# Kernel optimization log

Hardware: AMD Instinct MI355X
Metric: run time of the kernel (lower is better)

## Reference

```python
import jax, jax.numpy as jnp
import numpy as np

D_MODEL = 1024
N_HEADS = 16
SEQ = 2048
BATCH = 2


def setup_inputs() -> dict:
    key = jax.random.key(0)
    ks = jax.random.split(key, 12)
    s = 1.0 / np.sqrt(D_MODEL)
    return {
        "q_input": jax.random.normal(ks[0], (BATCH, SEQ, D_MODEL), jnp.float32),
        "k_input": jax.random.normal(ks[1], (BATCH, SEQ, D_MODEL), jnp.float32),
        "v_input": jax.random.normal(ks[2], (BATCH, SEQ, D_MODEL), jnp.float32),
        "key_padding_mask": jnp.zeros((BATCH, SEQ), dtype=bool),
        "wq": jax.random.normal(ks[3], (D_MODEL, D_MODEL), jnp.float32) * s,
        "bq": jnp.zeros((D_MODEL,), jnp.float32),
        "wk": jax.random.normal(ks[4], (D_MODEL, D_MODEL), jnp.float32) * s,
        "bk": jnp.zeros((D_MODEL,), jnp.float32),
        "wv": jax.random.normal(ks[5], (D_MODEL, D_MODEL), jnp.float32) * s,
        "bv": jnp.zeros((D_MODEL,), jnp.float32),
        "wo": jax.random.normal(ks[6], (D_MODEL, D_MODEL), jnp.float32) * s,
        "bo": jnp.zeros((D_MODEL,), jnp.float32),
    }


def reference(q_input, k_input, v_input, key_padding_mask, wq, bq, wk, bk, wv, bv, wo, bo):
    B, Lq, _ = q_input.shape
    Lk = k_input.shape[1]
    d_head = D_MODEL // N_HEADS
    # torch Linear: x @ W.T + b
    Q = q_input @ wq.T + bq
    K = k_input @ wk.T + bk
    V = v_input @ wv.T + bv
    # [B, H, L, d_head]
    Qh = Q.reshape(B, Lq, N_HEADS, d_head).transpose(0, 2, 1, 3)
    Kh = K.reshape(B, Lk, N_HEADS, d_head).transpose(0, 2, 1, 3)
    Vh = V.reshape(B, Lk, N_HEADS, d_head).transpose(0, 2, 1, 3)
    scores = jnp.einsum("bhqd,bhkd->bhqk", Qh, Kh) / jnp.sqrt(jnp.float32(d_head))
    # causal mask (use_mask=True)
    causal = jnp.arange(Lk)[None, :] > jnp.arange(Lq)[:, None]  # [Lq, Lk]
    scores = jnp.where(causal[None, None], -jnp.inf, scores)
    # key padding mask [B,1,1,Lk]
    scores = jnp.where(key_padding_mask[:, None, None, :], -jnp.inf, scores)
    # module's global all-inf fallback (scalar condition)
    probs = jnp.where(
        jnp.all(jnp.isinf(scores)),
        jnp.full_like(scores, 1.0 / Lk),
        jax.nn.softmax(scores, axis=-1),
    )
    # dropout is identity in eval mode
    out = jnp.einsum("bhqk,bhkd->bhqd", probs, Vh)
    out = out.transpose(0, 2, 1, 3).reshape(B, Lq, D_MODEL)
    return out @ wo.T + bo
```

## Files before the change

### kernel.cpp

```cpp
#include <hip/hip_runtime.h>
#include <cstdint>
#include <cstddef>

#define DM   1024
#define HEADS 16
#define DH    64
#define SEQL  2048
#define BATCH 2
#define MTOT  (BATCH*SEQL)

typedef __attribute__((ext_vector_type(8))) short short8;
typedef __attribute__((ext_vector_type(4))) float floatx4;

__device__ __forceinline__ unsigned short f2bf(float f) {
  unsigned int u = __float_as_uint(f);
  u = (u + 0x7FFFu + ((u >> 16) & 1u)) >> 16;
  return (unsigned short)u;
}

__device__ __forceinline__ void async_ld16(const void* g, void* l) {
  __builtin_amdgcn_global_load_lds(
      (const __attribute__((address_space(1))) unsigned int*)g,
      (__attribute__((address_space(3))) unsigned int*)l, 16, 0, 0);
}

__global__ void cvt_all(const float* __restrict__ q, const float* __restrict__ k,
                        const float* __restrict__ v, const float* __restrict__ w0,
                        const float* __restrict__ w1, const float* __restrict__ w2,
                        const float* __restrict__ w3,
                        unsigned short* __restrict__ Xq, unsigned short* __restrict__ Xk,
                        unsigned short* __restrict__ Xv, unsigned short* __restrict__ W0,
                        unsigned short* __restrict__ W1, unsigned short* __restrict__ W2,
                        unsigned short* __restrict__ W3) {
  const int bid = blockIdx.x;
  const float* src; unsigned short* dst; int base;
  if (bid < 12288) {
    int seg = bid >> 12;
    base = (bid & 4095) * 1024;
    src = seg == 0 ? q : seg == 1 ? k : v;
    dst = seg == 0 ? Xq : seg == 1 ? Xk : Xv;
  } else {
    int b2 = bid - 12288;
    int seg = b2 >> 10;
    base = (b2 & 1023) * 1024;
    src = seg == 0 ? w0 : seg == 1 ? w1 : seg == 2 ? w2 : w3;
    dst = seg == 0 ? W0 : seg == 1 ? W1 : seg == 2 ? W2 : W3;
  }
  int i = base + threadIdx.x * 4;
  float4 vv = *(const float4*)(src + i);
  ushort4 o;
  o.x = f2bf(vv.x); o.y = f2bf(vv.y); o.z = f2bf(vv.z); o.w = f2bf(vv.w);
  *(ushort4*)(dst + i) = o;
}

__global__ __launch_bounds__(256, 3) void qkv_gemm(
    const unsigned short* Xq, const unsigned short* Xk, const unsigned short* Xv,
    const unsigned short* Wq, const unsigned short* Wk, const unsigned short* Wv,
    const float* bq, const float* bk, const float* bv,
    unsigned short* Qo, unsigned short* Ko, unsigned short* VTo) {
  __shared__ unsigned short As[128 * 64], Bs[128 * 64];
  const unsigned short *A, *Bw; const float* bias; unsigned short* Cout;
  if (blockIdx.z == 0)      { A = Xq; Bw = Wq; bias = bq; Cout = Qo; }
  else if (blockIdx.z == 1) { A = Xk; Bw = Wk; bias = bk; Cout = Ko; }
  else                      { A = Xv; Bw = Wv; bias = bv; Cout = VTo; }

  const int K = DM, N = DM;
  const int m0 = blockIdx.y * 128, n0 = blockIdx.x * 128;
  const int tid  = threadIdx.x;
  const int lane = tid & 63, wvi = tid >> 6;
  const int lq = lane & 15, quad = lane >> 4;
  const int wrow = wvi >> 1, wcol = wvi & 1;

  floatx4 acc[4][4];
  #pragma unroll
  for (int i = 0; i < 4; i++)
    #pragma unroll
    for (int j = 0; j < 4; j++)
      #pragma unroll
      for (int e = 0; e < 4; e++) acc[i][j][e] = 0.0f;

  for (int kt = 0; kt < K; kt += 64) {
    #pragma unroll
    for (int cc = 0; cc < 4; cc++) {
      int c = wvi + cc * 4;
      int e = c * 512 + lane * 8;
      int r = e >> 6, col = e & 63;
      async_ld16(A  + (size_t)(m0 + r) * K + kt + col, As + c * 512);
      async_ld16(Bw + (size_t)(n0 + r) * K + kt + col, Bs + c * 512);
    }
    __syncthreads();
    #pragma unroll
    for (int ks = 0; ks < 64; ks += 32) {
      short8 af[4], bf[4];
      #pragma unroll
      for (int i = 0; i < 4; i++)
        af[i] = *(const short8*)&As[(wrow * 64 + i * 16 + lq) * 64 + ks + quad * 8];
      #pragma unroll
      for (int j = 0; j < 4; j++)
        bf[j] = *(const short8*)&Bs[(wcol * 64 + j * 16 + lq) * 64 + ks + quad * 8];
      #pragma unroll
      for (int i = 0; i < 4; i++)
        #pragma unroll
        for (int j = 0; j < 4; j++)
          acc[i][j] = __builtin_amdgcn_mfma_f32_16x16x32_bf16(af[i], bf[j], acc[i][j], 0, 0, 0);
    }
    __syncthreads();
  }

  if (blockIdx.z == 2) {
    #pragma unroll
    for (int i = 0; i < 4; i++) {
      const int rowg = m0 + wrow * 64 + i * 16 + quad * 4;
      const int bb  = rowg >> 11;
      const int kt2 = (rowg & 2047) >> 6;
      const int k0  = rowg & 63;
      #pragma unroll
      for (int j = 0; j < 4; j++) {
        const int colg = n0 + wcol * 64 + j * 16 + lq;
        const int h2 = colg >> 6, d2 = colg & 63;
        const float bb_v = bias[colg];
        ushort4 w;
        w.x = f2bf(acc[i][j][0] + bb_v);
        w.y = f2bf(acc[i][j][1] + bb_v);
        w.z = f2bf(acc[i][j][2] + bb_v);
        w.w = f2bf(acc[i][j][3] + bb_v);
        *(ushort4*)(Cout + (size_t)((bb * HEADS + h2) * 32 + kt2) * 4096 + d2 * 64 + k0) = w;
      }
    }
  } else {
    #pragma unroll
    for (int i = 0; i < 4; i++) {
      #pragma unroll
      for (int j = 0; j < 4; j++) {
        int colg = n0 + wcol * 64 + j * 16 + lq;
        float bb = bias[colg];
        #pragma unroll
        for (int r = 0; r < 4; r++) {
          int rowg = m0 + wrow * 64 + i * 16 + quad * 4 + r;
          Cout[(size_t)rowg * N + colg] = f2bf(acc[i][j][r] + bb);
        }
      }
    }
  }
}

__global__ __launch_bounds__(256, 4) void out_gemm(
    const unsigned short* __restrict__ A, const unsigned short* __restrict__ Bw,
    const float* __restrict__ bias, float* __restrict__ C) {
  __shared__ unsigned short As[128 * 64], Bs[64 * 64];
  const int K = DM, N = DM;
  const int m0 = blockIdx.y * 128, n0 = blockIdx.x * 64;
  const int tid  = threadIdx.x;
  const int lane = tid & 63, wvi = tid >> 6;
  const int lq = lane & 15, quad = lane >> 4;
  const int wrow = wvi >> 1, wcol = wvi & 1;

  floatx4 acc[4][2];
  #pragma unroll
  for (int i = 0; i < 4; i++)
    #pragma unroll
    for (int j = 0; j < 2; j++)
      #pragma unroll
      for (int e = 0; e < 4; e++) acc[i][j][e] = 0.0f;

  for (int kt = 0; kt < K; kt += 64) {
    #pragma unroll
    for (int cc = 0; cc < 4; cc++) {
      int c = wvi + cc * 4;
      int e = c * 512 + lane * 8;
      int r = e >> 6, col = e & 63;
      async_ld16(A + (size_t)(m0 + r) * K + kt + col, As + c * 512);
    }
    #pragma unroll
    for (int cc = 0; cc < 2; cc++) {
      int c = wvi + cc * 4;
      int e = c * 512 + lane * 8;
      int r = e >> 6, col = e & 63;
      async_ld16(Bw + (size_t)(n0 + r) * K + kt + col, Bs + c * 512);
    }
    __syncthreads();
    #pragma unroll
    for (int ks = 0; ks < 64; ks += 32) {
      short8 af[4], bf[2];
      #pragma unroll
      for (int i = 0; i < 4; i++)
        af[i] = *(const short8*)&As[(wrow * 64 + i * 16 + lq) * 64 + ks + quad * 8];
      #pragma unroll
      for (int j = 0; j < 2; j++)
        bf[j] = *(const short8*)&Bs[(wcol * 32 + j * 16 + lq) * 64 + ks + quad * 8];
      #pragma unroll
      for (int i = 0; i < 4; i++)
        #pragma unroll
        for (int j = 0; j < 2; j++)
          acc[i][j] = __builtin_amdgcn_mfma_f32_16x16x32_bf16(af[i], bf[j], acc[i][j], 0, 0, 0);
    }
    __syncthreads();
  }

  #pragma unroll
  for (int i = 0; i < 4; i++) {
    #pragma unroll
    for (int j = 0; j < 2; j++) {
      int colg = n0 + wcol * 32 + j * 16 + lq;
      float bb = bias[colg];
      #pragma unroll
      for (int r = 0; r < 4; r++) {
        int rowg = m0 + wrow * 64 + i * 16 + quad * 4 + r;
        C[(size_t)rowg * N + colg] = acc[i][j][r] + bb;
      }
    }
  }
}

__global__ __launch_bounds__(256, 4) void attn_kernel(
    const unsigned short* __restrict__ Q, const unsigned short* __restrict__ K,
    const unsigned short* __restrict__ VT, const unsigned char* __restrict__ kpm,
    unsigned short* __restrict__ O) {
  __shared__ unsigned short Ks[64 * 72];
  __shared__ unsigned short VTs[64 * 72];
  __shared__ unsigned short Ps[4][16 * 72];

  const int bid = blockIdx.x;
  const int g = bid >> 5;
  const int qt = (g < 8) ? (15 - g) : (g - 8);
  const int bh = bid & 31;
  const int h = bh & 15, b = bh >> 4;
  const int tid = threadIdx.x, lane = tid & 63, wvi = tid >> 6;
  const int lq = lane & 15, quad = lane >> 4;
  const size_t bbase = (size_t)b * SEQL * DM;

  const int srow = tid >> 4;
  const int scol = (tid & 15) * 4;

  const unsigned short* kptr = K + bbase + (size_t)h * DH + (size_t)srow * DM + scol;
  const unsigned short* vptr = VT + (size_t)(b * HEADS + h) * 32 * 4096 + srow * 64 + scol;
  const unsigned char*  mptr = kpm + (size_t)b * SEQL + quad * 4;

  const unsigned short* QrowA = Q + bbase + (size_t)(qt * 128 + wvi * 16 + lq) * DM + h * DH;
  const short8 qfA0 = *(const short8*)(QrowA + quad * 8);
  const short8 qfA1 = *(const short8*)(QrowA + 32 + quad * 8);
  const unsigned short* QrowB = QrowA + (size_t)64 * DM;
  const short8 qfB0 = *(const short8*)(QrowB + quad * 8);
  const short8 qfB1 = *(const short8*)(QrowB + 32 + quad * 8);

  const int nk = 2 * qt + 2;

  ushort4 kr[4], vr[4];
  unsigned int mr[4];
  #pragma unroll
  for (int j = 0; j < 4; j++) {
    kr[j] = *(const ushort4*)(kptr + (size_t)j * 16 * DM);
    vr[j] = *(const ushort4*)(vptr + j * 1024);
  }
  #pragma unroll
  for (int t = 0; t < 4; t++) mr[t] = *(const unsigned int*)(mptr + t * 16);
  kptr += (size_t)64 * DM; vptr += 4096; mptr += 64;

  float lA = 0.f, lB = 0.f;
  floatx4 oA[4], oB[4];
  #pragma unroll
  for (int t = 0; t < 4; t++)
    #pragma unroll
    for (int e = 0; e < 4; e++) { oA[t][e] = 0.f; oB[t][e] = 0.f; }

  const float SC = 0.125f * 1.44269504088896f;
  const float C0 = -24.0f * SC;
  const int qg = wvi * 16 + lq;

  for (int kt = 0; kt < nk; kt++) {
    __syncthreads();
    #pragma unroll
    for (int j = 0; j < 4; j++) {
      *(ushort4*)&Ks [(j * 16 + srow) * 72 + scol] = kr[j];
      *(ushort4*)&VTs[(j * 16 + srow) * 72 + scol] = vr[j];
    }
    unsigned int mcur[4];
    #pragma unroll
    for (int t = 0; t < 4; t++) mcur[t] = mr[t];
    __syncthreads();

    if (kt + 1 < nk) {
      #pragma unroll
      for (int j = 0; j < 4; j++) {
        kr[j] = *(const ushort4*)(kptr + (size_t)j * 16 * DM);
        vr[j] = *(const ushort4*)(vptr + j * 1024);
      }
      #pragma unroll
      for (int t = 0; t < 4; t++) mr[t] = *(const unsigned int*)(mptr + t * 16);
      kptr += (size_t)64 * DM; vptr += 4096; mptr += 64;
    }

    floatx4 sA[4], sB[4];
    #pragma unroll
    for (int t = 0; t < 4; t++) {
      #pragma unroll
      for (int e = 0; e < 4; e++) { sA[t][e] = 0.f; sB[t][e] = 0.f; }
      const short8 a0 = *(const short8*)&Ks[(t * 16 + lq) * 72 + quad * 8];
      const short8 a1 = *(const short8*)&Ks[(t * 16 + lq) * 72 + 32 + quad * 8];
      sA[t] = __builtin_amdgcn_mfma_f32_16x16x32_bf16(a0, qfA0, sA[t], 0, 0, 0);
      sA[t] = __builtin_amdgcn_mfma_f32_16x16x32_bf16(a1, qfA1, sA[t], 0, 0, 0);
      sB[t] = __builtin_amdgcn_mfma_f32_16x16x32_bf16(a0, qfB0, sB[t], 0, 0, 0);
      sB[t] = __builtin_amdgcn_mfma_f32_16x16x32_bf16(a1, qfB1, sB[t], 0, 0, 0);
    }

    if (__any((int)((mcur[0] | mcur[1] | mcur[2] | mcur[3]) != 0u))) {
      #pragma unroll
      for (int t = 0; t < 4; t++)
        #pragma unroll
        for (int r = 0; r < 4; r++)
          if ((mcur[t] >> (8 * r)) & 0xffu) { sA[t][r] = -1e33f; sB[t][r] = -1e33f; }
    }
    if (kt >= 2 * qt) {
      const int offA = qg + (2 * qt - kt) * 64;
      #pragma unroll
      for (int t = 0; t < 4; t++)
        #pragma unroll
        for (int r = 0; r < 4; r++)
          if (t * 16 + quad * 4 + r > offA) sA[t][r] = -1e33f;
    }
    if (kt == 2 * qt + 1) {
      #pragma unroll
      for (int t = 0; t < 4; t++)
        #pragma unroll
        for (int r = 0; r < 4; r++)
          if (t * 16 + quad * 4 + r > qg) sB[t][r] = -1e33f;
    }

    #pragma unroll
    for (int t = 0; t < 4; t++)
      #pragma unroll
      for (int r = 0; r < 4; r++) {
        const float pA = exp2f(fmaf(sA[t][r], SC, C0));
        const float pB = exp2f(fmaf(sB[t][r], SC, C0));
        sA[t][r] = pA; lA += pA;
        sB[t][r] = pB; lB += pB;
      }

    #pragma unroll
    for (int t = 0; t < 4; t++) {
      unsigned int p01 = (__float_as_uint(sA[t][1]) & 0xffff0000u) | (__float_as_uint(sA[t][0]) >> 16);
      unsigned int p23 = (__float_as_uint(sA[t][3]) & 0xffff0000u) | (__float_as_uint(sA[t][2]) >> 16);
      *(uint2*)&Ps[wvi][lq * 72 + t * 16 + quad * 4] = make_uint2(p01, p23);
    }
    const short8 paA0 = *(const short8*)&Ps[wvi][lq * 72 + quad * 8];
    const short8 paA1 = *(const short8*)&Ps[wvi][lq * 72 + 32 + quad * 8];
    #pragma unroll
    for (int t = 0; t < 4; t++) {
      unsigned int p01 = (__float_as_uint(sB[t][1]) & 0xffff0000u) | (__float_as_uint(sB[t][0]) >> 16);
      unsigned int p23 = (__float_as_uint(sB[t][3]) & 0xffff0000u) | (__float_as_uint(sB[t][2]) >> 16);
      *(uint2*)&Ps[wvi][lq * 72 + t * 16 + quad * 4] = make_uint2(p01, p23);
    }
    const short8 paB0 = *(const short8*)&Ps[wvi][lq * 72 + quad * 8];
    const short8 paB1 = *(const short8*)&Ps[wvi][lq * 72 + 32 + quad * 8];

    #pragma unroll
    for (int t = 0; t < 4; t++) {
      const short8 b0 = *(const short8*)&VTs[(t * 16 + lq) * 72 + quad * 8];
      const short8 b1 = *(const short8*)&VTs[(t * 16 + lq) * 72 + 32 + quad * 8];
      oA[t] = __builtin_amdgcn_mfma_f32_16x16x32_bf16(paA0, b0, oA[t], 0, 0, 0);
      oA[t] = __builtin_amdgcn_mfma_f32_16x16x32_bf16(paA1, b1, oA[t], 0, 0, 0);
      oB[t] = __builtin_amdgcn_mfma_f32_16x16x32_bf16(paB0, b0, oB[t], 0, 0, 0);
      oB[t] = __builtin_amdgcn_mfma_f32_16x16x32_bf16(paB1, b1, oB[t], 0, 0, 0);
    }
  }

  lA += __shfl_xor(lA, 16); lA += __shfl_xor(lA, 32);
  lB += __shfl_xor(lB, 16); lB += __shfl_xor(lB, 32);
  const float liA = 1.0f / lA, liB = 1.0f / lB;
  float invA[4], invB[4];
  #pragma unroll
  for (int r = 0; r < 4; r++) {
    invA[r] = __shfl(liA, quad * 20 + r);
    invB[r] = __shfl(liB, quad * 20 + r);
  }
  #pragma unroll
  for (int t = 0; t < 4; t++)
    #pragma unroll
    for (int r = 0; r < 4; r++) {
      const int rowA = qt * 128 + wvi * 16 + quad * 4 + r;
      const int colg = h * 64 + t * 16 + lq;
      O[bbase + (size_t)rowA * DM + colg] = f2bf(oA[t][r] * invA[r]);
      O[bbase + (size_t)(rowA + 64) * DM + colg] = f2bf(oB[t][r] * invB[r]);
    }
}

extern "C" void kernel_launch(void* const* d_in, const int* in_sizes, int n_in,
                              void* d_out, int out_size, void* d_ws, size_t ws_size,
                              hipStream_t stream) {
  const float* qin = (const float*)d_in[0];
  const float* kin = (const float*)d_in[1];
  const float* vin = (const float*)d_in[2];
  const unsigned char* kpm = (const unsigned char*)d_in[3];
  const float* wq = (const float*)d_in[4];
  const float* bq = (const float*)d_in[5];
  const float* wk = (const float*)d_in[6];
  const float* bk = (const float*)d_in[7];
  const float* wv = (const float*)d_in[8];
  const float* bv = (const float*)d_in[9];
  const float* wo = (const float*)d_in[10];
  const float* bo = (const float*)d_in[11];

  const size_t XN = (size_t)MTOT * DM;
  const size_t WN = (size_t)DM * DM;
  unsigned short* Xq  = (unsigned short*)d_ws;
  unsigned short* Xk  = Xq  + XN;
  unsigned short* Xv  = Xk  + XN;
  unsigned short* Wqb = Xv  + XN;
  unsigned short* Wkb = Wqb + WN;
  unsigned short* Wvb = Wkb + WN;
  unsigned short* Wob = Wvb + WN;
  unsigned short* Qb  = Wob + WN;
  unsigned short* Kb  = Qb  + XN;
  unsigned short* VTg = Kb  + XN;
  unsigned short* Ob  = VTg + XN;

  cvt_all<<<dim3(16384), 256, 0, stream>>>(qin, kin, vin, wq, wk, wv, wo,
                                           Xq, Xk, Xv, Wqb, Wkb, Wvb, Wob);

  dim3 g1(DM / 128, MTOT / 128, 3);
  qkv_gemm<<<g1, 256, 0, stream>>>(Xq, Xk, Xv, Wqb, Wkb, Wvb, bq, bk, bv, Qb, Kb, VTg);

  attn_kernel<<<dim3(BATCH * HEADS * (SEQL / 128)), 256, 0, stream>>>(Qb, Kb, VTg, kpm, Ob);

  dim3 g2(DM / 64, MTOT / 128, 1);
  out_gemm<<<g2, 256, 0, stream>>>(Ob, Wob, bo, (float*)d_out);
}
```

Before: 247.6 us.

## Pair mirrored causal query tiles per block to balance and skip masked work

Each attention block now handles two 64-row query tiles, j and 31-j, instead of two adjacent tiles. Every block therefore does the same total number of key tiles, and for key tiles past the first query tile's diagonal only the second tile's QK, softmax and PV are computed. Before, both halves always ran the full 2*qt+2 key tiles, including fully masked work. The launch bound drops to 2 blocks per SM and a second P scratch buffer is added, which may affect occupancy and register allocation.

```diff
diff --git a/kernel.cpp b/kernel.cpp
--- a/kernel.cpp
+++ b/kernel.cpp
@@ -212,17 +212,18 @@
   }
 }
 
-__global__ __launch_bounds__(256, 4) void attn_kernel(
+__global__ __launch_bounds__(256, 2) void attn_kernel(
     const unsigned short* __restrict__ Q, const unsigned short* __restrict__ K,
     const unsigned short* __restrict__ VT, const unsigned char* __restrict__ kpm,
     unsigned short* __restrict__ O) {
   __shared__ unsigned short Ks[64 * 72];
   __shared__ unsigned short VTs[64 * 72];
-  __shared__ unsigned short Ps[4][16 * 72];
+  __shared__ unsigned short PsA[4][16 * 72];
+  __shared__ unsigned short PsB[4][16 * 72];
 
   const int bid = blockIdx.x;
-  const int g = bid >> 5;
-  const int qt = (g < 8) ? (15 - g) : (g - 8);
+  const int j = bid >> 5;
+  const int qtA = j, qtB = 31 - j;
   const int bh = bid & 31;
   const int h = bh & 15, b = bh >> 4;
   const int tid = threadIdx.x, lane = tid & 63, wvi = tid >> 6;
@@ -236,21 +237,21 @@
   const unsigned short* vptr = VT + (size_t)(b * HEADS + h) * 32 * 4096 + srow * 64 + scol;
   const unsigned char*  mptr = kpm + (size_t)b * SEQL + quad * 4;
 
-  const unsigned short* QrowA = Q + bbase + (size_t)(qt * 128 + wvi * 16 + lq) * DM + h * DH;
+  const unsigned short* QrowA = Q + bbase + (size_t)(qtA * 64 + wvi * 16 + lq) * DM + h * DH;
   const short8 qfA0 = *(const short8*)(QrowA + quad * 8);
   const short8 qfA1 = *(const short8*)(QrowA + 32 + quad * 8);
-  const unsigned short* QrowB = QrowA + (size_t)64 * DM;
+  const unsigned short* QrowB = Q + bbase + (size_t)(qtB * 64 + wvi * 16 + lq) * DM + h * DH;
   const short8 qfB0 = *(const short8*)(QrowB + quad * 8);
   const short8 qfB1 = *(const short8*)(QrowB + 32 + quad * 8);
 
-  const int nk = 2 * qt + 2;
+  const int nk = qtB + 1;
 
   ushort4 kr[4], vr[4];
   unsigned int mr[4];
   #pragma unroll
-  for (int j = 0; j < 4; j++) {
-    kr[j] = *(const ushort4*)(kptr + (size_t)j * 16 * DM);
-    vr[j] = *(const ushort4*)(vptr + j * 1024);
+  for (int jj = 0; jj < 4; jj++) {
+    kr[jj] = *(const ushort4*)(kptr + (size_t)jj * 16 * DM);
+    vr[jj] = *(const ushort4*)(vptr + jj * 1024);
   }
   #pragma unroll
   for (int t = 0; t < 4; t++) mr[t] = *(const unsigned int*)(mptr + t * 16);
@@ -270,9 +271,9 @@
   for (int kt = 0; kt < nk; kt++) {
     __syncthreads();
     #pragma unroll
-    for (int j = 0; j < 4; j++) {
-      *(ushort4*)&Ks [(j * 16 + srow) * 72 + scol] = kr[j];
-      *(ushort4*)&VTs[(j * 16 + srow) * 72 + scol] = vr[j];
+    for (int jj = 0; jj < 4; jj++) {
+      *(ushort4*)&Ks [(jj * 16 + srow) * 72 + scol] = kr[jj];
+      *(ushort4*)&VTs[(jj * 16 + srow) * 72 + scol] = vr[jj];
     }
     unsigned int mcur[4];
     #pragma unroll
@@ -281,44 +282,58 @@
 
     if (kt + 1 < nk) {
       #pragma unroll
-      for (int j = 0; j < 4; j++) {
-        kr[j] = *(const ushort4*)(kptr + (size_t)j * 16 * DM);
-        vr[j] = *(const ushort4*)(vptr + j * 1024);
+      for (int jj = 0; jj < 4; jj++) {
+        kr[jj] = *(const ushort4*)(kptr + (size_t)jj * 16 * DM);
+        vr[jj] = *(const ushort4*)(vptr + jj * 1024);
       }
       #pragma unroll
       for (int t = 0; t < 4; t++) mr[t] = *(const unsigned int*)(mptr + t * 16);
       kptr += (size_t)64 * DM; vptr += 4096; mptr += 64;
     }
 
+    const bool dual = (kt <= qtA);
+    const bool anym = __any((int)((mcur[0] | mcur[1] | mcur[2] | mcur[3]) != 0u));
+
     floatx4 sA[4], sB[4];
-    #pragma unroll
-    for (int t = 0; t < 4; t++) {
-      #pragma unroll
-      for (int e = 0; e < 4; e++) { sA[t][e] = 0.f; sB[t][e] = 0.f; }
-      const short8 a0 = *(const short8*)&Ks[(t * 16 + lq) * 72 + quad * 8];
-      const short8 a1 = *(const short8*)&Ks[(t * 16 + lq) * 72 + 32 + quad * 8];
-      sA[t] = __builtin_amdgcn_mfma_f32_16x16x32_bf16(a0, qfA0, sA[t], 0, 0, 0);
-      sA[t] = __builtin_amdgcn_mfma_f32_16x16x32_bf16(a1, qfA1, sA[t], 0, 0, 0);
-      sB[t] = __builtin_amdgcn_mfma_f32_16x16x32_bf16(a0, qfB0, sB[t], 0, 0, 0);
-      sB[t] = __builtin_amdgcn_mfma_f32_16x16x32_bf16(a1, qfB1, sB[t], 0, 0, 0);
-    }
-
-    if (__any((int)((mcur[0] | mcur[1] | mcur[2] | mcur[3]) != 0u))) {
+    if (dual) {
+      #pragma unroll
+      for (int t = 0; t < 4; t++) {
+        #pragma unroll
+        for (int e = 0; e < 4; e++) { sA[t][e] = 0.f; sB[t][e] = 0.f; }
+        const short8 a0 = *(const short8*)&Ks[(t * 16 + lq) * 72 + quad * 8];
+        const short8 a1 = *(const short8*)&Ks[(t * 16 + lq) * 72 + 32 + quad * 8];
+        sA[t] = __builtin_amdgcn_mfma_f32_16x16x32_bf16(a0, qfA0, sA[t], 0, 0, 0);
+        sA[t] = __builtin_amdgcn_mfma_f32_16x16x32_bf16(a1, qfA1, sA[t], 0, 0, 0);
+        sB[t] = __builtin_amdgcn_mfma_f32_16x16x32_bf16(a0, qfB0, sB[t], 0, 0, 0);
+        sB[t] = __builtin_amdgcn_mfma_f32_16x16x32_bf16(a1, qfB1, sB[t], 0, 0, 0);
+      }
+    } else {
+      #pragma unroll
+      for (int t = 0; t < 4; t++) {
+        #pragma unroll
+        for (int e = 0; e < 4; e++) sB[t][e] = 0.f;
+        const short8 a0 = *(const short8*)&Ks[(t * 16 + lq) * 72 + quad * 8];
+        const short8 a1 = *(const short8*)&Ks[(t * 16 + lq) * 72 + 32 + quad * 8];
+        sB[t] = __builtin_amdgcn_mfma_f32_16x16x32_bf16(a0, qfB0, sB[t], 0, 0, 0);
+        sB[t] = __builtin_amdgcn_mfma_f32_16x16x32_bf16(a1, qfB1, sB[t], 0, 0, 0);
+      }
+    }
+
+    if (anym) {
       #pragma unroll
       for (int t = 0; t < 4; t++)
         #pragma unroll
         for (int r = 0; r < 4; r++)
-          if ((mcur[t] >> (8 * r)) & 0xffu) { sA[t][r] = -1e33f; sB[t][r] = -1e33f; }
-    }
-    if (kt >= 2 * qt) {
-      const int offA = qg + (2 * qt - kt) * 64;
+          if ((mcur[t] >> (8 * r)) & 0xffu) { sB[t][r] = -1e33f; if (dual) sA[t][r] = -1e33f; }
+    }
+    if (dual && kt == qtA) {
       #pragma unroll
       for (int t = 0; t < 4; t++)
         #pragma unroll
         for (int r = 0; r < 4; r++)
-          if (t * 16 + quad * 4 + r > offA) sA[t][r] = -1e33f;
-    }
-    if (kt == 2 * qt + 1) {
+          if (t * 16 + quad * 4 + r > qg) sA[t][r] = -1e33f;
+    }
+    if (kt == qtB) {
       #pragma unroll
       for (int t = 0; t < 4; t++)
         #pragma unroll
@@ -330,37 +345,53 @@
     for (int t = 0; t < 4; t++)
       #pragma unroll
       for (int r = 0; r < 4; r++) {
-        const float pA = exp2f(fmaf(sA[t][r], SC, C0));
         const float pB = exp2f(fmaf(sB[t][r], SC, C0));
-        sA[t][r] = pA; lA += pA;
         sB[t][r] = pB; lB += pB;
       }
-
-    #pragma unroll
-    for (int t = 0; t < 4; t++) {
-      unsigned int p01 = (__float_as_uint(sA[t][1]) & 0xffff0000u) | (__float_as_uint(sA[t][0]) >> 16);
-      unsigned int p23 = (__float_as_uint(sA[t][3]) & 0xffff0000u) | (__float_as_uint(sA[t][2]) >> 16);
-      *(uint2*)&Ps[wvi][lq * 72 + t * 16 + quad * 4] = make_uint2(p01, p23);
-    }
-    const short8 paA0 = *(const short8*)&Ps[wvi][lq * 72 + quad * 8];
-    const short8 paA1 = *(const short8*)&Ps[wvi][lq * 72 + 32 + quad * 8];
     #pragma unroll
     for (int t = 0; t < 4; t++) {
       unsigned int p01 = (__float_as_uint(sB[t][1]) & 0xffff0000u) | (__float_as_uint(sB[t][0]) >> 16);
       unsigned int p23 = (__float_as_uint(sB[t][3]) & 0xffff0000u) | (__float_as_uint(sB[t][2]) >> 16);
-      *(uint2*)&Ps[wvi][lq * 72 + t * 16 + quad * 4] = make_uint2(p01, p23);
-    }
-    const short8 paB0 = *(const short8*)&Ps[wvi][lq * 72 + quad * 8];
-    const short8 paB1 = *(const short8*)&Ps[wvi][lq * 72 + 32 + quad * 8];
-
-    #pragma unroll
-    for (int t = 0; t < 4; t++) {
-      const short8 b0 = *(const short8*)&VTs[(t * 16 + lq) * 72 + quad * 8];
-      const short8 b1 = *(const short8*)&VTs[(t * 16 + lq) * 72 + 32 + quad * 8];
-      oA[t] = __builtin_amdgcn_mfma_f32_16x16x32_bf16(paA0, b0, oA[t], 0, 0, 0);
-      oA[t] = __builtin_amdgcn_mfma_f32_16x16x32_bf16(paA1, b1, oA[t], 0, 0, 0);
-      oB[t] = __builtin_amdgcn_mfma_f32_16x16x32_bf16(paB0, b0, oB[t], 0, 0, 0);
-      oB[t] = __builtin_amdgcn_mfma_f32_16x16x32_bf16(paB1, b1, oB[t], 0, 0, 0);
+      *(uint2*)&PsB[wvi][lq * 72 + t * 16 + quad * 4] = make_uint2(p01, p23);
+    }
+    if (dual) {
+      #pragma unroll
+      for (int t = 0; t < 4; t++)
+        #pragma unroll
+        for (int r = 0; r < 4; r++) {
+          const float pA = exp2f(fmaf(sA[t][r], SC, C0));
+          sA[t][r] = pA; lA += pA;
+        }
+      #pragma unroll
+      for (int t = 0; t < 4; t++) {
+        unsigned int p01 = (__float_as_uint(sA[t][1]) & 0xffff0000u) | (__float_as_uint(sA[t][0]) >> 16);
+        unsigned int p23 = (__float_as_uint(sA[t][3]) & 0xffff0000u) | (__float_as_uint(sA[t][2]) >> 16);
+        *(uint2*)&PsA[wvi][lq * 72 + t * 16 + quad * 4] = make_uint2(p01, p23);
+      }
+    }
+
+    const short8 paB0 = *(const short8*)&PsB[wvi][lq * 72 + quad * 8];
+    const short8 paB1 = *(const short8*)&PsB[wvi][lq * 72 + 32 + quad * 8];
+    if (dual) {
+      const short8 paA0 = *(const short8*)&PsA[wvi][lq * 72 + quad * 8];
+      const short8 paA1 = *(const short8*)&PsA[wvi][lq * 72 + 32 + quad * 8];
+      #pragma unroll
+      for (int t = 0; t < 4; t++) {
+        const short8 b0 = *(const short8*)&VTs[(t * 16 + lq) * 72 + quad * 8];
+        const short8 b1 = *(const short8*)&VTs[(t * 16 + lq) * 72 + 32 + quad * 8];
+        oA[t] = __builtin_amdgcn_mfma_f32_16x16x32_bf16(paA0, b0, oA[t], 0, 0, 0);
+        oA[t] = __builtin_amdgcn_mfma_f32_16x16x32_bf16(paA1, b1, oA[t], 0, 0, 0);
+        oB[t] = __builtin_amdgcn_mfma_f32_16x16x32_bf16(paB0, b0, oB[t], 0, 0, 0);
+        oB[t] = __builtin_amdgcn_mfma_f32_16x16x32_bf16(paB1, b1, oB[t], 0, 0, 0);
+      }
+    } else {
+      #pragma unroll
+      for (int t = 0; t < 4; t++) {
+        const short8 b0 = *(const short8*)&VTs[(t * 16 + lq) * 72 + quad * 8];
+        const short8 b1 = *(const short8*)&VTs[(t * 16 + lq) * 72 + 32 + quad * 8];
+        oB[t] = __builtin_amdgcn_mfma_f32_16x16x32_bf16(paB0, b0, oB[t], 0, 0, 0);
+        oB[t] = __builtin_amdgcn_mfma_f32_16x16x32_bf16(paB1, b1, oB[t], 0, 0, 0);
+      }
     }
   }
 
@@ -377,10 +408,11 @@
   for (int t = 0; t < 4; t++)
     #pragma unroll
     for (int r = 0; r < 4; r++) {
-      const int rowA = qt * 128 + wvi * 16 + quad * 4 + r;
+      const int rowA = qtA * 64 + wvi * 16 + quad * 4 + r;
+      const int rowB = qtB * 64 + wvi * 16 + quad * 4 + r;
       const int colg = h * 64 + t * 16 + lq;
       O[bbase + (size_t)rowA * DM + colg] = f2bf(oA[t][r] * invA[r]);
-      O[bbase + (size_t)(rowA + 64) * DM + colg] = f2bf(oB[t][r] * invB[r]);
+      O[bbase + (size_t)rowB * DM + colg] = f2bf(oB[t][r] * invB[r]);
     }
 }
 
@@ -420,7 +452,7 @@
   dim3 g1(DM / 128, MTOT / 128, 3);
   qkv_gemm<<<g1, 256, 0, stream>>>(Xq, Xk, Xv, Wqb, Wkb, Wvb, bq, bk, bv, Qb, Kb, VTg);
 
-  attn_kernel<<<dim3(BATCH * HEADS * (SEQL / 128)), 256, 0, stream>>>(Qb, Kb, VTg, kpm, Ob);
+  attn_kernel<<<dim3(BATCH * HEADS * 16), 256, 0, stream>>>(Qb, Kb, VTg, kpm, Ob);
 
   dim3 g2(DM / 64, MTOT / 128, 1);
   out_gemm<<<g2, 256, 0, stream>>>(Ob, Wob, bo, (float*)d_out);
```

After: 232.2 us. 6.2% less time.
